# Kernel tuning notes

Hardware: AMD Instinct MI355X
Metric: run time of the kernel (lower is better)

Reference implementation:

```python
import jax, jax.numpy as jnp
import numpy as np

N_SAMPLE = 128
POS_MAX = 32            # n_sample * pos_ratio = 128 * 0.25
POS_THR = 0.5
NEG_HI = 0.5
NEG_LO = 0.0
EPS = np.float32(np.finfo(np.float32).eps)
IMG_SIZE = 800.0


def _make_boxes(key, shape):
    # well-formed corner boxes: x1<x2, y1<y2, inside image
    k1, k2 = jax.random.split(key)
    xy = jax.random.uniform(k1, shape[:-1] + (2,)) * (IMG_SIZE - 50.0)
    wh = jax.random.uniform(k2, shape[:-1] + (2,)) * 300.0 + 1.0
    return jnp.concatenate([xy, jnp.minimum(xy + wh, IMG_SIZE)], axis=-1)


def setup_inputs() -> dict:
    key = jax.random.key(0)
    k1, k2, k3, k4 = jax.random.split(key, 4)
    roi = _make_boxes(k1, (32, 6000, 4))          # [B, R, 4]
    gt_boxes = _make_boxes(k2, (32, 100, 4))      # [B, G, 4]
    labels = jax.random.randint(k3, (32, 100), 1, 81, dtype=jnp.int32)  # [B, G]
    image = jax.random.normal(k4, (32, 3, 224, 224), dtype=jnp.float32)
    return {"roi": roi, "gt_boxes": gt_boxes, "labels": labels, "image": image}


def _iou_matrix(roi, gt):
    # roi [R,4], gt [G,4] -> [R,G]
    ix1 = jnp.maximum(roi[:, None, 0], gt[None, :, 0])
    iy1 = jnp.maximum(roi[:, None, 1], gt[None, :, 1])
    ix2 = jnp.minimum(roi[:, None, 2], gt[None, :, 2])
    iy2 = jnp.minimum(roi[:, None, 3], gt[None, :, 3])
    iw = jnp.maximum(ix2 - ix1, 0.0)
    ih = jnp.maximum(iy2 - iy1, 0.0)
    inter = iw * ih
    area_r = (roi[:, 2] - roi[:, 0]) * (roi[:, 3] - roi[:, 1])
    area_g = (gt[:, 2] - gt[:, 0]) * (gt[:, 3] - gt[:, 1])
    return inter / (area_r[:, None] + area_g[None, :] - inter)


def _rank_desc(score):
    return jnp.argsort(jnp.argsort(-score))


def _per_image(roi, gt, labels, key):
    # roi [R,4], gt [G,4], labels [G]
    ious = _iou_matrix(roi, gt)                       # [R,G]
    gt_assignment = jnp.argmax(ious, axis=1)          # [R]
    max_iou = jnp.max(ious, axis=1)                   # [R]

    pos_mask = max_iou >= POS_THR
    neg_mask = (max_iou < NEG_HI) & (max_iou >= NEG_LO)

    # random priorities emulate np.random.choice without replacement
    r = jax.random.uniform(key, (roi.shape[0],), minval=1e-6, maxval=1.0)
    pos_rank = _rank_desc(jnp.where(pos_mask, r, -1.0))
    is_sel_pos = pos_mask & (pos_rank < POS_MAX)      # min(POS_MAX, n_pos) positives
    n_pos = jnp.sum(is_sel_pos)
    neg_rank = _rank_desc(jnp.where(neg_mask, r, -1.0))
    is_sel_neg = neg_mask & (neg_rank < (N_SAMPLE - n_pos))

    # positives first (prio 2+r), then negatives (1+r), rest excluded
    prio = jnp.where(is_sel_pos, 2.0 + r, jnp.where(is_sel_neg, 1.0 + r, r - 10.0))
    vals, keep = jax.lax.top_k(prio, N_SAMPLE)        # keep [128]
    valid = vals >= 1.0
    kept_pos = is_sel_pos[keep]

    gt_roi_labels = jnp.where(kept_pos, labels[gt_assignment[keep]], 0)

    sample_roi = jnp.where(valid[:, None], roi[keep], 0.0)   # [128,4]
    base = gt[gt_assignment[keep]]                            # [128,4]

    w = jnp.maximum(roi[keep, 2] - roi[keep, 0], EPS)
    h = jnp.maximum(roi[keep, 3] - roi[keep, 1], EPS)
    cx = roi[keep, 0] + 0.5 * (roi[keep, 2] - roi[keep, 0])
    cy = roi[keep, 1] + 0.5 * (roi[keep, 3] - roi[keep, 1])
    bw = base[:, 2] - base[:, 0]
    bh = base[:, 3] - base[:, 1]
    bcx = base[:, 0] + 0.5 * bw
    bcy = base[:, 1] + 0.5 * bh

    dx = (bcx - cx) / w
    dy = (bcy - cy) / h
    dw = jnp.log(bw / w)
    dh = jnp.log(bh / h)
    deltas = jnp.where(valid[:, None], jnp.stack([dx, dy, dw, dh], axis=1), 0.0)
    return sample_roi, gt_roi_labels, deltas


def reference(roi, gt_boxes, labels, image):
    # image only used for visualization in the original; no math depends on it.
    B = roi.shape[0]
    keys = jax.random.split(jax.random.key(42), B)
    sample_roi, gt_roi_labels, gt_roi_bbox = jax.vmap(_per_image)(roi, gt_boxes, labels, keys)
    return sample_roi, gt_roi_labels, gt_roi_bbox
```

## Files before the change

kernel.cpp:

```cpp
#include <hip/hip_runtime.h>
#include <stdint.h>

#pragma clang fp contract(off)

#define B_IMG 32
#define R_N   6000
#define G_N   100
#define NS    128
#define PMAX  32
#define NBUCK 1024
#define BCAP  512
#define SEL_T 1024

#ifndef JAX_PARTITIONABLE
#define JAX_PARTITIONABLE 1
#endif

__device__ __forceinline__ uint32_t rotl32(uint32_t v, int d) {
  return (v << d) | (v >> (32 - d));
}

__device__ __forceinline__ void tf2x32(uint32_t k0, uint32_t k1,
                                       uint32_t x0, uint32_t x1,
                                       uint32_t& o0, uint32_t& o1) {
  const uint32_t k2 = k0 ^ k1 ^ 0x1BD11BDAu;
  x0 += k0; x1 += k1;
#define TF_R(r) { x0 += x1; x1 = rotl32(x1, r); x1 ^= x0; }
  TF_R(13) TF_R(15) TF_R(26) TF_R(6)
  x0 += k1; x1 += k2 + 1u;
  TF_R(17) TF_R(29) TF_R(16) TF_R(24)
  x0 += k2; x1 += k0 + 2u;
  TF_R(13) TF_R(15) TF_R(26) TF_R(6)
  x0 += k0; x1 += k1 + 3u;
  TF_R(17) TF_R(29) TF_R(16) TF_R(24)
  x0 += k1; x1 += k2 + 4u;
  TF_R(13) TF_R(15) TF_R(26) TF_R(6)
  x0 += k2; x1 += k0 + 5u;
#undef TF_R
  o0 = x0; o1 = x1;
}

__device__ __forceinline__ float tf_uniform(uint32_t bits) {
#pragma clang fp contract(off)
  float f = __uint_as_float((bits >> 9) | 0x3f800000u) - 1.0f;
  float r = f * (1.0f - 1e-6f) + 1e-6f;
  return fmaxf(1e-6f, r);
}

__global__ __launch_bounds__(256) void prep_kernel(
    const float* __restrict__ roi, const float* __restrict__ gt,
    float* __restrict__ wr, float* __restrict__ wmiou, int* __restrict__ wgta) {
#pragma clang fp contract(off)
  const int b = blockIdx.y;
  const int i = blockIdx.x * 256 + threadIdx.x;

  __shared__ float sg[G_N * 4];
  __shared__ float sga[G_N];
  for (int t = threadIdx.x; t < G_N * 4; t += 256) sg[t] = gt[b * G_N * 4 + t];
  __syncthreads();
  if (threadIdx.x < G_N) {
    int g = threadIdx.x;
    sga[g] = (sg[g * 4 + 2] - sg[g * 4 + 0]) * (sg[g * 4 + 3] - sg[g * 4 + 1]);
  }
  __syncthreads();
  if (i >= R_N) return;

  const float* rp = roi + ((size_t)b * R_N + i) * 4;
  float x1 = rp[0], y1 = rp[1], x2 = rp[2], y2 = rp[3];
  float ar = (x2 - x1) * (y2 - y1);

  float best = -1.0f; int bi = 0;
  for (int g = 0; g < G_N; ++g) {
    float gx1 = sg[g * 4 + 0], gy1 = sg[g * 4 + 1];
    float gx2 = sg[g * 4 + 2], gy2 = sg[g * 4 + 3];
    float ix1 = fmaxf(x1, gx1), iy1 = fmaxf(y1, gy1);
    float ix2 = fminf(x2, gx2), iy2 = fminf(y2, gy2);
    float iw = fmaxf(ix2 - ix1, 0.0f);
    float ih = fmaxf(iy2 - iy1, 0.0f);
    float inter = iw * ih;
    float denom = (ar + sga[g]) - inter;
    float iou = inter / denom;
    if (iou > best) { best = iou; bi = g; }
  }

  uint32_t bits;
#if JAX_PARTITIONABLE
  uint32_t kb0, kb1;
  tf2x32(0u, 42u, 0u, (uint32_t)b, kb0, kb1);
  uint32_t t0, t1;
  tf2x32(kb0, kb1, 0u, (uint32_t)i, t0, t1);
  bits = t0 ^ t1;
#else
  uint32_t kb0, kb1, d0, d1;
  if (b < 16) {
    tf2x32(0u, 42u, (uint32_t)(2 * b),     (uint32_t)(2 * b + 32), kb0, d0);
    tf2x32(0u, 42u, (uint32_t)(2 * b + 1), (uint32_t)(2 * b + 33), kb1, d1);
  } else {
    int c = b - 16;
    tf2x32(0u, 42u, (uint32_t)(2 * c),     (uint32_t)(2 * c + 32), d0, kb0);
    tf2x32(0u, 42u, (uint32_t)(2 * c + 1), (uint32_t)(2 * c + 33), d1, kb1);
  }
  uint32_t t0, t1;
  if (i < R_N / 2) { tf2x32(kb0, kb1, (uint32_t)i, (uint32_t)(i + R_N / 2), t0, t1); bits = t0; }
  else             { tf2x32(kb0, kb1, (uint32_t)(i - R_N / 2), (uint32_t)i, t0, t1); bits = t1; }
#endif

  size_t o = (size_t)b * R_N + i;
  wr[o] = tf_uniform(bits);
  wmiou[o] = best;
  wgta[o] = bi;
}

__global__ __launch_bounds__(SEL_T) void select_kernel(
    const float* __restrict__ roi, const float* __restrict__ gt,
    const int* __restrict__ labels,
    const float* __restrict__ wr, const float* __restrict__ wmiou,
    const int* __restrict__ wgta, float* __restrict__ out) {
#pragma clang fp contract(off)
  const int b = blockIdx.x;
  const int tid = threadIdx.x;

  __shared__ float sr[R_N];
  __shared__ unsigned char scls[R_N];
  __shared__ unsigned char ssel[R_N];
  __shared__ int S[NBUCK];
  __shared__ int sh_cntpos;
  __shared__ int sh_B, sh_A;
  __shared__ int candIdx[BCAP];
  __shared__ int candCnt;
  __shared__ int posList[PMAX];
  __shared__ int negList[NS];
  __shared__ int listCnt[2];
  __shared__ int outIdx[NS];

  if (tid == 0) sh_cntpos = 0;
  if (tid < 2) listCnt[tid] = 0;
  __syncthreads();

  int mycnt = 0;
  for (int i = tid; i < R_N; i += SEL_T) {
    sr[i] = wr[(size_t)b * R_N + i];
    unsigned char p = (wmiou[(size_t)b * R_N + i] >= 0.5f) ? 1 : 0;
    scls[i] = p;
    ssel[i] = 0;
    mycnt += p;
  }
  if (mycnt) atomicAdd(&sh_cntpos, mycnt);
  __syncthreads();

  const int cntPos = sh_cntpos;
  const int cntNeg = R_N - cntPos;
  const int nPosSel = min(cntPos, PMAX);
  const int Kneg = NS - nPosSel;

  for (int c = 1; c >= 0; --c) {
    const int quota = (c == 1) ? PMAX : Kneg;
    const int cnt   = (c == 1) ? cntPos : cntNeg;
    if (cnt <= quota) {
      for (int i = tid; i < R_N; i += SEL_T)
        if (scls[i] == (unsigned char)c) ssel[i] = 1;
      __syncthreads();
      continue;
    }
    if (tid < NBUCK) S[tid] = 0;
    if (tid == 0) candCnt = 0;
    __syncthreads();
    for (int i = tid; i < R_N; i += SEL_T)
      if (scls[i] == (unsigned char)c) {
        int bk = min((int)(sr[i] * (float)NBUCK), NBUCK - 1);
        atomicAdd(&S[bk], 1);
      }
    __syncthreads();
    for (int off = 1; off < NBUCK; off <<= 1) {
      int v = 0;
      if (tid < NBUCK && tid + off < NBUCK) v = S[tid + off];
      __syncthreads();
      if (tid < NBUCK) S[tid] += v;
      __syncthreads();
    }
    if (tid < NBUCK) {
      int Sh = S[tid];
      int Sn = (tid + 1 < NBUCK) ? S[tid + 1] : 0;
      if (Sh >= quota && Sn < quota) { sh_B = tid; sh_A = Sn; }
    }
    __syncthreads();
    const int Bb = sh_B, A = sh_A;
    for (int i = tid; i < R_N; i += SEL_T)
      if (scls[i] == (unsigned char)c) {
        int bk = min((int)(sr[i] * (float)NBUCK), NBUCK - 1);
        if (bk > Bb) ssel[i] = 1;
        else if (bk == Bb) {
          int p = atomicAdd(&candCnt, 1);
          if (p < BCAP) candIdx[p] = i;
        }
      }
    __syncthreads();
    const int M = candCnt;
    if (M <= BCAP) {
      if (tid < M) {
        int i = candIdx[tid];
        float ri = sr[i];
        int beats = 0;
        for (int u = 0; u < M; ++u) {
          int j = candIdx[u];
          float rj = sr[j];
          if (rj > ri || (rj == ri && j < i)) beats++;
        }
        if (A + beats < quota) ssel[i] = 1;
      }
    } else {
      for (int i = tid; i < R_N; i += SEL_T)
        if (scls[i] == (unsigned char)c) {
          int bk = min((int)(sr[i] * (float)NBUCK), NBUCK - 1);
          if (bk == Bb) {
            float ri = sr[i];
            int beats = 0;
            for (int j = 0; j < R_N; ++j)
              if (scls[j] == (unsigned char)c) {
                float rj = sr[j];
                int bj = min((int)(rj * (float)NBUCK), NBUCK - 1);
                if (bj == Bb && (rj > ri || (rj == ri && j < i))) beats++;
              }
            if (A + beats < quota) ssel[i] = 1;
          }
        }
    }
    __syncthreads();
  }

  for (int i = tid; i < R_N; i += SEL_T)
    if (ssel[i]) {
      if (scls[i]) { int p = atomicAdd(&listCnt[1], 1); if (p < PMAX) posList[p] = i; }
      else         { int p = atomicAdd(&listCnt[0], 1); if (p < NS)   negList[p] = i; }
    }
  __syncthreads();
  const int nP = min(listCnt[1], PMAX);
  const int nN = min(listCnt[0], NS);

  if (tid < NS) outIdx[tid] = -1;
  __syncthreads();

  if (tid < nP) {
    int i = posList[tid];
    float pr = 2.0f + sr[i];
    int slot = 0;
    for (int u = 0; u < nP; ++u) {
      int j = posList[u];
      float pj = 2.0f + sr[j];
      if (pj > pr || (pj == pr && j < i)) slot++;
    }
    outIdx[slot] = i;
  }
  if (tid < nN) {
    int i = negList[tid];
    float pr = 1.0f + sr[i];
    int slot = 0;
    for (int u = 0; u < nN; ++u) {
      int j = negList[u];
      float pj = 1.0f + sr[j];
      if (pj > pr || (pj == pr && j < i)) slot++;
    }
    outIdx[nP + slot] = i;
  }
  __syncthreads();

  if (tid < NS) {
    const int p = tid;
    const int i = outIdx[p];
    float o_roi[4] = {0.f, 0.f, 0.f, 0.f};
    float o_lab = 0.f;
    float o_d[4] = {0.f, 0.f, 0.f, 0.f};
    if (i >= 0) {
      const float* rp = roi + ((size_t)b * R_N + i) * 4;
      float x1 = rp[0], y1 = rp[1], x2 = rp[2], y2 = rp[3];
      o_roi[0] = x1; o_roi[1] = y1; o_roi[2] = x2; o_roi[3] = y2;
      int g = wgta[(size_t)b * R_N + i];
      const float* gp = gt + ((size_t)b * G_N + g) * 4;
      float gx1 = gp[0], gy1 = gp[1], gx2 = gp[2], gy2 = gp[3];
      if (scls[i]) o_lab = (float)labels[b * G_N + g];
      const float EPSF = 1.1920928955078125e-7f;
      float w = fmaxf(x2 - x1, EPSF);
      float h = fmaxf(y2 - y1, EPSF);
      float cx = x1 + 0.5f * (x2 - x1);
      float cy = y1 + 0.5f * (y2 - y1);
      float bw = gx2 - gx1, bh = gy2 - gy1;
      float bcx = gx1 + 0.5f * bw, bcy = gy1 + 0.5f * bh;
      o_d[0] = (bcx - cx) / w;
      o_d[1] = (bcy - cy) / h;
      o_d[2] = logf(bw / w);
      o_d[3] = logf(bh / h);
    }
    float* out0 = out;
    float* out1 = out + (size_t)B_IMG * NS * 4;
    float* out2 = out1 + (size_t)B_IMG * NS;
    const int base = b * NS + p;
    out0[base * 4 + 0] = o_roi[0];
    out0[base * 4 + 1] = o_roi[1];
    out0[base * 4 + 2] = o_roi[2];
    out0[base * 4 + 3] = o_roi[3];
    out1[base] = o_lab;
    out2[base * 4 + 0] = o_d[0];
    out2[base * 4 + 1] = o_d[1];
    out2[base * 4 + 2] = o_d[2];
    out2[base * 4 + 3] = o_d[3];
  }
}

extern "C" void kernel_launch(void* const* d_in, const int* in_sizes, int n_in,
                              void* d_out, int out_size, void* d_ws, size_t ws_size,
                              hipStream_t stream) {
  const float* roi    = (const float*)d_in[0];
  const float* gt     = (const float*)d_in[1];
  const int*   labels = (const int*)d_in[2];

  float* wr    = (float*)d_ws;
  float* wmiou = wr + (size_t)B_IMG * R_N;
  int*   wgta  = (int*)(wmiou + (size_t)B_IMG * R_N);

  dim3 g1((R_N + 255) / 256, B_IMG);
  prep_kernel<<<g1, 256, 0, stream>>>(roi, gt, wr, wmiou, wgta);
  select_kernel<<<B_IMG, SEL_T, 0, stream>>>(roi, gt, labels, wr, wmiou, wgta,
                                             (float*)d_out);
}
```

Baseline: 107.3 us.

## Encode class in sign of random score and histogram both classes in one pass

Prep now writes one signed score per ROI, whose sign marks the positive class, and drops the separate max-IoU buffer. It also computes the per-image Threefry key once per block and uses float4 loads for ROI and GT boxes. The select kernel keeps eight scores per thread in registers, builds both class histograms in a single pass, and replaces the barrier-per-step suffix scan with a wave-shuffle scan. It then gathers selected indices and ranks boundary candidates for both classes at the same time, reading cached values instead of large shared arrays. The aim is to cut global traffic, shared memory and barrier count, at the cost of more register pressure and a fallback path that rereads global memory.

```diff
diff --git a/kernel.cpp b/kernel.cpp
--- a/kernel.cpp
+++ b/kernel.cpp
@@ -11,6 +11,8 @@
 #define NBUCK 1024
 #define BCAP  512
 #define SEL_T 1024
+#define T_LOAD 750
+#define NITEM 8
 
 #ifndef JAX_PARTITIONABLE
 #define JAX_PARTITIONABLE 1
@@ -49,14 +51,24 @@
 
 __global__ __launch_bounds__(256) void prep_kernel(
     const float* __restrict__ roi, const float* __restrict__ gt,
-    float* __restrict__ wr, float* __restrict__ wmiou, int* __restrict__ wgta) {
+    float* __restrict__ wr, int* __restrict__ wgta) {
 #pragma clang fp contract(off)
   const int b = blockIdx.y;
   const int i = blockIdx.x * 256 + threadIdx.x;
 
-  __shared__ float sg[G_N * 4];
+  __shared__ __align__(16) float sg[G_N * 4];
   __shared__ float sga[G_N];
-  for (int t = threadIdx.x; t < G_N * 4; t += 256) sg[t] = gt[b * G_N * 4 + t];
+#if JAX_PARTITIONABLE
+  __shared__ uint32_t skb[2];
+#endif
+  for (int t = threadIdx.x; t < G_N * 4; t += 256) sg[t] = gt[(size_t)b * G_N * 4 + t];
+#if JAX_PARTITIONABLE
+  if (threadIdx.x == 0) {
+    uint32_t a, c;
+    tf2x32(0u, 42u, 0u, (uint32_t)b, a, c);
+    skb[0] = a; skb[1] = c;
+  }
+#endif
   __syncthreads();
   if (threadIdx.x < G_N) {
     int g = threadIdx.x;
@@ -65,16 +77,15 @@
   __syncthreads();
   if (i >= R_N) return;
 
-  const float* rp = roi + ((size_t)b * R_N + i) * 4;
-  float x1 = rp[0], y1 = rp[1], x2 = rp[2], y2 = rp[3];
+  const float4 rb = *(const float4*)(roi + ((size_t)b * R_N + i) * 4);
+  float x1 = rb.x, y1 = rb.y, x2 = rb.z, y2 = rb.w;
   float ar = (x2 - x1) * (y2 - y1);
 
   float best = -1.0f; int bi = 0;
   for (int g = 0; g < G_N; ++g) {
-    float gx1 = sg[g * 4 + 0], gy1 = sg[g * 4 + 1];
-    float gx2 = sg[g * 4 + 2], gy2 = sg[g * 4 + 3];
-    float ix1 = fmaxf(x1, gx1), iy1 = fmaxf(y1, gy1);
-    float ix2 = fminf(x2, gx2), iy2 = fminf(y2, gy2);
+    const float4 gv = ((const float4*)sg)[g];
+    float ix1 = fmaxf(x1, gv.x), iy1 = fmaxf(y1, gv.y);
+    float ix2 = fminf(x2, gv.z), iy2 = fminf(y2, gv.w);
     float iw = fmaxf(ix2 - ix1, 0.0f);
     float ih = fmaxf(iy2 - iy1, 0.0f);
     float inter = iw * ih;
@@ -85,10 +96,8 @@
 
   uint32_t bits;
 #if JAX_PARTITIONABLE
-  uint32_t kb0, kb1;
-  tf2x32(0u, 42u, 0u, (uint32_t)b, kb0, kb1);
   uint32_t t0, t1;
-  tf2x32(kb0, kb1, 0u, (uint32_t)i, t0, t1);
+  tf2x32(skb[0], skb[1], 0u, (uint32_t)i, t0, t1);
   bits = t0 ^ t1;
 #else
   uint32_t kb0, kb1, d0, d1;
@@ -105,179 +114,207 @@
   else             { tf2x32(kb0, kb1, (uint32_t)(i - R_N / 2), (uint32_t)i, t0, t1); bits = t1; }
 #endif
 
+  float r = tf_uniform(bits);
   size_t o = (size_t)b * R_N + i;
-  wr[o] = tf_uniform(bits);
-  wmiou[o] = best;
+  wr[o] = (best >= 0.5f) ? -r : r;
   wgta[o] = bi;
 }
 
 __global__ __launch_bounds__(SEL_T) void select_kernel(
     const float* __restrict__ roi, const float* __restrict__ gt,
     const int* __restrict__ labels,
-    const float* __restrict__ wr, const float* __restrict__ wmiou,
-    const int* __restrict__ wgta, float* __restrict__ out) {
+    const float* __restrict__ wr, const int* __restrict__ wgta,
+    float* __restrict__ out) {
 #pragma clang fp contract(off)
   const int b = blockIdx.x;
   const int tid = threadIdx.x;
-
-  __shared__ float sr[R_N];
-  __shared__ unsigned char scls[R_N];
-  __shared__ unsigned char ssel[R_N];
-  __shared__ int S[NBUCK];
-  __shared__ int sh_cntpos;
-  __shared__ int sh_B, sh_A;
-  __shared__ int candIdx[BCAP];
-  __shared__ int candCnt;
-  __shared__ int posList[PMAX];
-  __shared__ int negList[NS];
-  __shared__ int listCnt[2];
-  __shared__ int outIdx[NS];
-
-  if (tid == 0) sh_cntpos = 0;
-  if (tid < 2) listCnt[tid] = 0;
-  __syncthreads();
-
-  int mycnt = 0;
-  for (int i = tid; i < R_N; i += SEL_T) {
-    sr[i] = wr[(size_t)b * R_N + i];
-    unsigned char p = (wmiou[(size_t)b * R_N + i] >= 0.5f) ? 1 : 0;
-    scls[i] = p;
-    ssel[i] = 0;
-    mycnt += p;
-  }
-  if (mycnt) atomicAdd(&sh_cntpos, mycnt);
-  __syncthreads();
-
-  const int cntPos = sh_cntpos;
+  const int lane = tid & 63;
+  const int wid = tid >> 6;
+  const size_t base = (size_t)b * R_N;
+
+  __shared__ int S[2][NBUCK];
+  __shared__ __align__(16) float sgt[G_N * 4];
+  __shared__ int slab[G_N];
+  __shared__ int wsum[2][16];
+  __shared__ int bndB[2], bndA[2];
+  __shared__ int candN[2], listN[2];
+  __shared__ int   candI[2][BCAP];
+  __shared__ float candV[2][BCAP];
+  __shared__ int   posIdx[PMAX]; __shared__ float posR[PMAX];
+  __shared__ int   negIdx[NS];   __shared__ float negR[NS];
+  __shared__ int outIdxA[NS];
+
+  for (int t = tid; t < G_N * 4; t += SEL_T) sgt[t] = gt[(size_t)b * G_N * 4 + t];
+  for (int t = tid; t < G_N; t += SEL_T) slab[t] = labels[b * G_N + t];
+  for (int t = tid; t < 2 * NBUCK; t += SEL_T) ((int*)S)[t] = 0;
+  if (tid < 2) { candN[tid] = 0; listN[tid] = 0; }
+  __syncthreads();
+
+  float rv[NITEM]; int bk[NITEM]; int cl[NITEM];
+  if (tid < T_LOAD) {
+    const float4 a0 = *(const float4*)(wr + base + (size_t)tid * NITEM);
+    const float4 a1 = *(const float4*)(wr + base + (size_t)tid * NITEM + 4);
+    float s[NITEM] = { a0.x, a0.y, a0.z, a0.w, a1.x, a1.y, a1.z, a1.w };
+#pragma unroll
+    for (int k = 0; k < NITEM; ++k) {
+      float sv = s[k];
+      int c = (sv < 0.0f) ? 1 : 0;
+      float r = fabsf(sv);
+      rv[k] = r; cl[k] = c;
+      bk[k] = min((int)(r * (float)NBUCK), NBUCK - 1);
+      atomicAdd(&S[c][bk[k]], 1);
+    }
+  }
+  __syncthreads();
+
+  {
+    const int h = NBUCK - 1 - tid;
+    int vp = S[1][h], vn = S[0][h];
+#pragma unroll
+    for (int d = 1; d < 64; d <<= 1) {
+      int up = __shfl_up(vp, d);
+      int un = __shfl_up(vn, d);
+      if (lane >= d) { vp += up; vn += un; }
+    }
+    if (lane == 63) { wsum[1][wid] = vp; wsum[0][wid] = vn; }
+    __syncthreads();
+    int op = 0, on = 0;
+    for (int w = 0; w < wid; ++w) { op += wsum[1][w]; on += wsum[0][w]; }
+    S[1][h] = vp + op;
+    S[0][h] = vn + on;
+  }
+  __syncthreads();
+
+  const int cntPos = S[1][0];
+  const int nPosSel = (cntPos < PMAX) ? cntPos : PMAX;
+  const int qNeg = NS - nPosSel;
   const int cntNeg = R_N - cntPos;
-  const int nPosSel = min(cntPos, PMAX);
-  const int Kneg = NS - nPosSel;
-
-  for (int c = 1; c >= 0; --c) {
-    const int quota = (c == 1) ? PMAX : Kneg;
-    const int cnt   = (c == 1) ? cntPos : cntNeg;
-    if (cnt <= quota) {
-      for (int i = tid; i < R_N; i += SEL_T)
-        if (scls[i] == (unsigned char)c) ssel[i] = 1;
-      __syncthreads();
-      continue;
-    }
-    if (tid < NBUCK) S[tid] = 0;
-    if (tid == 0) candCnt = 0;
-    __syncthreads();
-    for (int i = tid; i < R_N; i += SEL_T)
-      if (scls[i] == (unsigned char)c) {
-        int bk = min((int)(sr[i] * (float)NBUCK), NBUCK - 1);
-        atomicAdd(&S[bk], 1);
+
+  if (tid == 0) {
+    if (cntPos <= PMAX) { bndB[1] = -1; bndA[1] = 0; }
+    if (cntNeg <= qNeg) { bndB[0] = -1; bndA[0] = 0; }
+  }
+  if (cntPos > PMAX) {
+    int Sh = S[1][tid];
+    int Sn = (tid + 1 < NBUCK) ? S[1][tid + 1] : 0;
+    if (Sh >= PMAX && Sn < PMAX) { bndB[1] = tid; bndA[1] = Sn; }
+  }
+  if (cntNeg > qNeg) {
+    int Sh = S[0][tid];
+    int Sn = (tid + 1 < NBUCK) ? S[0][tid + 1] : 0;
+    if (Sh >= qNeg && Sn < qNeg) { bndB[0] = tid; bndA[0] = Sn; }
+  }
+  __syncthreads();
+
+  if (tid < T_LOAD) {
+#pragma unroll
+    for (int k = 0; k < NITEM; ++k) {
+      const int i = tid * NITEM + k;
+      const int c = cl[k];
+      const int Bb = bndB[c];
+      if (bk[k] > Bb) {
+        if (c) { int p = atomicAdd(&listN[1], 1); if (p < PMAX) { posIdx[p] = i; posR[p] = rv[k]; } }
+        else   { int p = atomicAdd(&listN[0], 1); if (p < NS)   { negIdx[p] = i; negR[p] = rv[k]; } }
+      } else if (bk[k] == Bb) {
+        int p = atomicAdd(&candN[c], 1);
+        if (p < BCAP) { candI[c][p] = i; candV[c][p] = rv[k]; }
       }
-    __syncthreads();
-    for (int off = 1; off < NBUCK; off <<= 1) {
-      int v = 0;
-      if (tid < NBUCK && tid + off < NBUCK) v = S[tid + off];
-      __syncthreads();
-      if (tid < NBUCK) S[tid] += v;
-      __syncthreads();
-    }
-    if (tid < NBUCK) {
-      int Sh = S[tid];
-      int Sn = (tid + 1 < NBUCK) ? S[tid + 1] : 0;
-      if (Sh >= quota && Sn < quota) { sh_B = tid; sh_A = Sn; }
-    }
-    __syncthreads();
-    const int Bb = sh_B, A = sh_A;
-    for (int i = tid; i < R_N; i += SEL_T)
-      if (scls[i] == (unsigned char)c) {
-        int bk = min((int)(sr[i] * (float)NBUCK), NBUCK - 1);
-        if (bk > Bb) ssel[i] = 1;
-        else if (bk == Bb) {
-          int p = atomicAdd(&candCnt, 1);
-          if (p < BCAP) candIdx[p] = i;
-        }
+    }
+  }
+  __syncthreads();
+
+  {
+    const int c = (tid < 512) ? 1 : 0;
+    const int m = (tid < 512) ? tid : tid - 512;
+    const int M = candN[c];
+    if (M <= BCAP && m < M) {
+      const int i = candI[c][m]; const float ri = candV[c][m];
+      const int A = bndA[c];
+      const int q = c ? PMAX : qNeg;
+      int beats = 0;
+      for (int u = 0; u < M; ++u) {
+        float rj = candV[c][u]; int j = candI[c][u];
+        if (rj > ri || (rj == ri && j < i)) beats++;
       }
-    __syncthreads();
-    const int M = candCnt;
-    if (M <= BCAP) {
-      if (tid < M) {
-        int i = candIdx[tid];
-        float ri = sr[i];
-        int beats = 0;
-        for (int u = 0; u < M; ++u) {
-          int j = candIdx[u];
-          float rj = sr[j];
-          if (rj > ri || (rj == ri && j < i)) beats++;
-        }
-        if (A + beats < quota) ssel[i] = 1;
+      if (A + beats < q) {
+        if (c) { int p = atomicAdd(&listN[1], 1); if (p < PMAX) { posIdx[p] = i; posR[p] = ri; } }
+        else   { int p = atomicAdd(&listN[0], 1); if (p < NS)   { negIdx[p] = i; negR[p] = ri; } }
       }
-    } else {
-      for (int i = tid; i < R_N; i += SEL_T)
-        if (scls[i] == (unsigned char)c) {
-          int bk = min((int)(sr[i] * (float)NBUCK), NBUCK - 1);
-          if (bk == Bb) {
-            float ri = sr[i];
+    }
+  }
+#pragma unroll
+  for (int c = 0; c < 2; ++c) {
+    if (candN[c] > BCAP) {
+      const int q = c ? PMAX : qNeg;
+      const int A = bndA[c], Bb = bndB[c];
+      if (tid < T_LOAD) {
+#pragma unroll
+        for (int k = 0; k < NITEM; ++k) {
+          const int i = tid * NITEM + k;
+          if (cl[k] == c && bk[k] == Bb) {
+            const float ri = rv[k];
             int beats = 0;
-            for (int j = 0; j < R_N; ++j)
-              if (scls[j] == (unsigned char)c) {
-                float rj = sr[j];
+            for (int j = 0; j < R_N; ++j) {
+              float sj = wr[base + j];
+              int cj = (sj < 0.0f) ? 1 : 0;
+              if (cj == c) {
+                float rj = fabsf(sj);
                 int bj = min((int)(rj * (float)NBUCK), NBUCK - 1);
                 if (bj == Bb && (rj > ri || (rj == ri && j < i))) beats++;
               }
-            if (A + beats < quota) ssel[i] = 1;
+            }
+            if (A + beats < q) {
+              if (c) { int p = atomicAdd(&listN[1], 1); if (p < PMAX) { posIdx[p] = i; posR[p] = ri; } }
+              else   { int p = atomicAdd(&listN[0], 1); if (p < NS)   { negIdx[p] = i; negR[p] = ri; } }
+            }
           }
         }
-    }
-    __syncthreads();
-  }
-
-  for (int i = tid; i < R_N; i += SEL_T)
-    if (ssel[i]) {
-      if (scls[i]) { int p = atomicAdd(&listCnt[1], 1); if (p < PMAX) posList[p] = i; }
-      else         { int p = atomicAdd(&listCnt[0], 1); if (p < NS)   negList[p] = i; }
-    }
-  __syncthreads();
-  const int nP = min(listCnt[1], PMAX);
-  const int nN = min(listCnt[0], NS);
-
-  if (tid < NS) outIdx[tid] = -1;
+      }
+    }
+  }
+  __syncthreads();
+
+  const int nP = min(listN[1], PMAX);
+  const int nN = min(listN[0], NS);
+
+  if (tid < NS) outIdxA[tid] = -1;
   __syncthreads();
 
   if (tid < nP) {
-    int i = posList[tid];
-    float pr = 2.0f + sr[i];
+    const int i = posIdx[tid]; const float pr = 2.0f + posR[tid];
     int slot = 0;
     for (int u = 0; u < nP; ++u) {
-      int j = posList[u];
-      float pj = 2.0f + sr[j];
+      float pj = 2.0f + posR[u]; int j = posIdx[u];
       if (pj > pr || (pj == pr && j < i)) slot++;
     }
-    outIdx[slot] = i;
-  }
-  if (tid < nN) {
-    int i = negList[tid];
-    float pr = 1.0f + sr[i];
+    outIdxA[slot] = i;
+  }
+  if (tid >= 128 && (tid - 128) < nN) {
+    const int m = tid - 128;
+    const int i = negIdx[m]; const float pr = 1.0f + negR[m];
     int slot = 0;
     for (int u = 0; u < nN; ++u) {
-      int j = negList[u];
-      float pj = 1.0f + sr[j];
+      float pj = 1.0f + negR[u]; int j = negIdx[u];
       if (pj > pr || (pj == pr && j < i)) slot++;
     }
-    outIdx[nP + slot] = i;
+    outIdxA[nP + slot] = i;
   }
   __syncthreads();
 
   if (tid < NS) {
     const int p = tid;
-    const int i = outIdx[p];
-    float o_roi[4] = {0.f, 0.f, 0.f, 0.f};
+    const int i = outIdxA[p];
+    float4 o_roi = { 0.f, 0.f, 0.f, 0.f };
     float o_lab = 0.f;
-    float o_d[4] = {0.f, 0.f, 0.f, 0.f};
+    float4 o_d = { 0.f, 0.f, 0.f, 0.f };
     if (i >= 0) {
-      const float* rp = roi + ((size_t)b * R_N + i) * 4;
-      float x1 = rp[0], y1 = rp[1], x2 = rp[2], y2 = rp[3];
-      o_roi[0] = x1; o_roi[1] = y1; o_roi[2] = x2; o_roi[3] = y2;
-      int g = wgta[(size_t)b * R_N + i];
-      const float* gp = gt + ((size_t)b * G_N + g) * 4;
-      float gx1 = gp[0], gy1 = gp[1], gx2 = gp[2], gy2 = gp[3];
-      if (scls[i]) o_lab = (float)labels[b * G_N + g];
+      const float4 rr = *(const float4*)(roi + (base + (size_t)i) * 4);
+      float x1 = rr.x, y1 = rr.y, x2 = rr.z, y2 = rr.w;
+      o_roi = rr;
+      const int g = wgta[base + (size_t)i];
+      float gx1 = sgt[g * 4 + 0], gy1 = sgt[g * 4 + 1];
+      float gx2 = sgt[g * 4 + 2], gy2 = sgt[g * 4 + 3];
+      if (p < nP) o_lab = (float)slab[g];
       const float EPSF = 1.1920928955078125e-7f;
       float w = fmaxf(x2 - x1, EPSF);
       float h = fmaxf(y2 - y1, EPSF);
@@ -285,24 +322,18 @@
       float cy = y1 + 0.5f * (y2 - y1);
       float bw = gx2 - gx1, bh = gy2 - gy1;
       float bcx = gx1 + 0.5f * bw, bcy = gy1 + 0.5f * bh;
-      o_d[0] = (bcx - cx) / w;
-      o_d[1] = (bcy - cy) / h;
-      o_d[2] = logf(bw / w);
-      o_d[3] = logf(bh / h);
+      o_d.x = (bcx - cx) / w;
+      o_d.y = (bcy - cy) / h;
+      o_d.z = logf(bw / w);
+      o_d.w = logf(bh / h);
     }
     float* out0 = out;
     float* out1 = out + (size_t)B_IMG * NS * 4;
     float* out2 = out1 + (size_t)B_IMG * NS;
-    const int base = b * NS + p;
-    out0[base * 4 + 0] = o_roi[0];
-    out0[base * 4 + 1] = o_roi[1];
-    out0[base * 4 + 2] = o_roi[2];
-    out0[base * 4 + 3] = o_roi[3];
-    out1[base] = o_lab;
-    out2[base * 4 + 0] = o_d[0];
-    out2[base * 4 + 1] = o_d[1];
-    out2[base * 4 + 2] = o_d[2];
-    out2[base * 4 + 3] = o_d[3];
+    const int basei = b * NS + p;
+    *(float4*)(out0 + (size_t)basei * 4) = o_roi;
+    out1[basei] = o_lab;
+    *(float4*)(out2 + (size_t)basei * 4) = o_d;
   }
 }
 
@@ -313,12 +344,11 @@
   const float* gt     = (const float*)d_in[1];
   const int*   labels = (const int*)d_in[2];
 
-  float* wr    = (float*)d_ws;
-  float* wmiou = wr + (size_t)B_IMG * R_N;
-  int*   wgta  = (int*)(wmiou + (size_t)B_IMG * R_N);
+  float* wr   = (float*)d_ws;
+  int*   wgta = (int*)(wr + (size_t)B_IMG * R_N);
 
   dim3 g1((R_N + 255) / 256, B_IMG);
-  prep_kernel<<<g1, 256, 0, stream>>>(roi, gt, wr, wmiou, wgta);
-  select_kernel<<<B_IMG, SEL_T, 0, stream>>>(roi, gt, labels, wr, wmiou, wgta,
+  prep_kernel<<<g1, 256, 0, stream>>>(roi, gt, wr, wgta);
+  select_kernel<<<B_IMG, SEL_T, 0, stream>>>(roi, gt, labels, wr, wgta,
                                              (float*)d_out);
 }
```

Measured after the change: 98.43 us. -8.3%, faster.
